# Kernel tuning notes

Measured on AMD Instinct MI355X. Metric: run time of the kernel, lower is better.

The kernel has to match this reference:

```python
import jax, jax.numpy as jnp
import numpy as np

B, T, C, H = 4, 4096, 1024, 64


def setup_inputs() -> dict:
    key = jax.random.key(0)
    k1, k2, k3, k4 = jax.random.split(key, 4)
    x = jax.random.normal(k1, (B, T, C), dtype=jnp.float32)
    # nn.Linear(C, H, bias=False) weights, stored as [C, H] so y = x @ W
    Wq = jax.random.normal(k2, (C, H), dtype=jnp.float32) * (C ** -0.5)
    Wk = jax.random.normal(k3, (C, H), dtype=jnp.float32) * (C ** -0.5)
    Wv = jax.random.normal(k4, (C, H), dtype=jnp.float32) * (C ** -0.5)
    return {"x": x, "Wq": Wq, "Wk": Wk, "Wv": Wv}


def reference(x, Wq, Wk, Wv):
    # x: (B,T,C) -> q,k,v: (B,T,H)
    q = jnp.einsum('btc,ch->bth', x, Wq)
    k = jnp.einsum('btc,ch->bth', x, Wk)
    v = jnp.einsum('btc,ch->bth', x, Wv)
    scale = q.shape[-1] ** -0.5
    # (B,T,T) attention scores with causal mask
    scores = jnp.einsum('bqh,bkh->bqk', q, k) * scale
    t = x.shape[1]
    causal = jnp.tril(jnp.ones((t, t), dtype=bool))
    scores = jnp.where(causal, scores, -jnp.inf)
    attn = jax.nn.softmax(scores, axis=-1)
    return jnp.einsum('bqk,bkh->bqh', attn, v)
```

## Files before the change

### kernel.cpp

```cpp
#include <hip/hip_runtime.h>

#define BATCH 4
#define SEQ   4096
#define CDIM  1024
#define HDIM  64

typedef __attribute__((ext_vector_type(8))) short bf16x8;
typedef __attribute__((ext_vector_type(4))) float f32x4;

#define WT_OFF 0
#define Q_OFF  (3 * HDIM * CDIM)
#define KF_OFF (Q_OFF + BATCH * SEQ * HDIM)
#define VF_OFF (KF_OFF + BATCH * SEQ * HDIM)

static __device__ __forceinline__ short f2bf(float f) {
  union { float f; unsigned u; } a; a.f = f;
  unsigned r = a.u + 0x7fffu + ((a.u >> 16) & 1u);
  return (short)(r >> 16);
}

static __device__ __forceinline__ bf16x8 ld8(const short* p) {
  return *(const bf16x8*)p;
}

__global__ void wcvt_kernel(const float* __restrict__ wq, const float* __restrict__ wk,
                            const float* __restrict__ wv, short* __restrict__ wt2) {
  int idx = blockIdx.x * 256 + threadIdx.x;
  int m = idx >> 16;
  int f = idx & 65535;
  int k0g = f >> 11, hc = (f >> 9) & 3, lr = (f >> 5) & 15, lg = (f >> 3) & 3, j = f & 7;
  int c = k0g * 32 + lg * 8 + j, h = hc * 16 + lr;
  const float* w = (m == 0) ? wq : (m == 1) ? wk : wv;
  wt2[((k0g * 12 + m * 4 + hc) * 64 + lr * 4 + lg) * 8 + j] = f2bf(w[c * 64 + h]);
}

__global__ __launch_bounds__(512) void proj_kernel(const float* __restrict__ x,
                                                   const short* __restrict__ wt2,
                                                   short* __restrict__ ws) {
  __shared__ short xs[2][1024];
  __shared__ short k_lds[8][16][24];
  __shared__ short v_lds[8][16][24];

  int tid = threadIdx.x;
  int widx = tid >> 6, lane = tid & 63;
  int lr = lane & 15, lg = lane >> 4;
  int row0 = blockIdx.x * 32;
  int rbh = widx >> 2;
  int hcw = widx & 3;

  int srow = tid >> 4, sc2 = tid & 15;
  const float* xsrc = x + (size_t)(row0 + srow) * CDIM + sc2 * 2;
  int sdst = (srow >> 4) * 512 + (srow & 15) * 32 + (sc2 >> 2) * 8 + (sc2 & 3) * 2;

  const short* xrd  = &xs[0][0] + rbh * 512 + (lr * 4 + lg) * 8;
  const short* bptr = wt2 + (hcw * 64 + lr * 4 + lg) * 8;

  f32x4 acc[3] = {};

#define LDX(K)  (*(const float2*)(xsrc + (K) * 32))
#define STAGE(A, BUF) do {                                                   \
    unsigned u_ = (unsigned)(unsigned short)f2bf((A).x) |                    \
                  ((unsigned)(unsigned short)f2bf((A).y) << 16);             \
    *(unsigned*)(&xs[(BUF)][sdst]) = u_;                                     \
  } while (0)
#define COMPUTE(BUF, K) do {                                                 \
    bf16x8 af_ = *(const bf16x8*)(xrd + (BUF) * 1024);                       \
    const short* bk_ = bptr + (K) * (12 * 512);                              \
    _Pragma("unroll")                                                        \
    for (int pp = 0; pp < 3; ++pp) {                                         \
      bf16x8 bf_ = ld8(bk_ + pp * 2048);                                     \
      acc[pp] = __builtin_amdgcn_mfma_f32_16x16x32_bf16(af_, bf_, acc[pp], 0, 0, 0); \
    }                                                                        \
  } while (0)

  float2 a1 = LDX(1);
  { float2 a0 = LDX(0); STAGE(a0, 0); }
  __syncthreads();

  for (int k = 0; k < 32; k += 2) {
    float2 an0 = {0.f, 0.f}, an1 = {0.f, 0.f};
    if (k + 2 < 32) an0 = LDX(k + 2);
    COMPUTE(0, k);
    STAGE(a1, 1);
    __syncthreads();
    if (k + 2 < 32) an1 = LDX(k + 3);
    COMPUTE(1, k + 1);
    if (k + 2 < 32) STAGE(an0, 0);
    __syncthreads();
    a1 = an1;
  }

  short* qs  = ws + Q_OFF;
  short* kfr = ws + KF_OFF;
  short* vfr = ws + VF_OFF;
  int rbase = row0 + rbh * 16;
#pragma unroll
  for (int reg = 0; reg < 4; ++reg) {
    int t = rbase + lg * 4 + reg;
    qs[t * 64 + hcw * 16 + lr] = f2bf(acc[0][reg]);
    k_lds[widx][lg * 4 + reg][lr] = f2bf(acc[1][reg]);
    v_lds[widx][lr][lg * 4 + reg] = f2bf(acc[2][reg]);
  }
  int b = rbase >> 12;
  int tb = rbase & (SEQ - 1);
  int kb64 = tb >> 6, st = (tb >> 4) & 3;
  if (lane < 32) {
    int i0 = lane >> 1, f8 = (lane & 1) * 8;
    size_t kblk = ((((size_t)b * 64 + kb64) * 4 + st) * 2 + (hcw >> 1)) * 512;
    bf16x8 kv8 = *(const bf16x8*)(&k_lds[widx][i0][f8]);
    *(bf16x8*)(kfr + kblk + ((hcw & 1) * 2 + (f8 >> 3)) * 128 + i0 * 8) = kv8;
    size_t vblk = ((((size_t)b * 64 + kb64) * 2 + ((tb >> 5) & 1)) * 4 + hcw) * 512;
    bf16x8 vv8 = *(const bf16x8*)(&v_lds[widx][i0][f8]);
    *(bf16x8*)(vfr + vblk + (((tb & 16) + f8) >> 3) * 128 + i0 * 8) = vv8;
  }
}

__global__ __launch_bounds__(512, 4) void attn_kernel(const short* __restrict__ ws,
                                                      float* __restrict__ out) {
  __shared__ float p_o[8][4][4][64];
  __shared__ float p_l[8][4][64];
  __shared__ short plds[8][16][72];

  int widx = threadIdx.x >> 6, lane = threadIdx.x & 63;
  int lr = lane & 15, lg = lane >> 4;
  int g = blockIdx.x;

  const short* qs  = ws + Q_OFF;
  const short* kfr = ws + KF_OFF;
  const short* vfr = ws + VF_OFF;
  short* myp = &plds[widx][0][0];

  for (int tt = 0; tt < 2; ++tt) {
    int j = tt == 0 ? g : 1023 - g;
    int t16 = 255 - (j >> 2), b = j & 3;
    int qrow0 = b * SEQ + t16 * 16;
    int nkv = (t16 >> 2) + 1;

    bf16x8 qf0 = ld8(qs + (qrow0 + lr) * 64 + lg * 8);
    bf16x8 qf1 = ld8(qs + (qrow0 + lr) * 64 + 32 + lg * 8);
    const short* kb_b = kfr + (size_t)b * 64 * 4096 + lane * 8;
    const short* vb_b = vfr + (size_t)b * 64 * 4096 + lane * 8;

    f32x4 o[4] = {};
    float l_run[4] = {};

    if (tt) __syncthreads();

    bf16x8 kf[8];
    int kvb = widx;
    if (kvb < nkv) {
      const short* kb = kb_b + (size_t)kvb * 4096;
#pragma unroll
      for (int q8 = 0; q8 < 8; ++q8) kf[q8] = ld8(kb + q8 * 512);
    }

    for (; kvb < nkv; kvb += 8) {
      int kv0 = kvb * 64;

      f32x4 s[4] = {};
#pragma unroll
      for (int st = 0; st < 4; ++st) {
        s[st] = __builtin_amdgcn_mfma_f32_16x16x32_bf16(qf0, kf[st * 2],     s[st], 0, 0, 0);
        s[st] = __builtin_amdgcn_mfma_f32_16x16x32_bf16(qf1, kf[st * 2 + 1], s[st], 0, 0, 0);
      }

      bf16x8 vv[8];
      {
        const short* vb = vb_b + (size_t)kvb * 4096;
#pragma unroll
        for (int q8 = 0; q8 < 8; ++q8) vv[q8] = ld8(vb + q8 * 512);
      }
      int kvn = kvb + 8;
      if (kvn < nkv) {
        const short* kb = kb_b + (size_t)kvn * 4096;
#pragma unroll
        for (int q8 = 0; q8 < 8; ++q8) kf[q8] = ld8(kb + q8 * 512);
      }

      bool last = (kvb == nkv - 1);
#pragma unroll
      for (int reg = 0; reg < 4; ++reg) {
        int ig = t16 * 16 + lg * 4 + reg;
#pragma unroll
        for (int st = 0; st < 4; ++st) {
          float v = s[st][reg] * 0.125f;
          if (last && (kv0 + st * 16 + lr > ig)) v = -1e30f;
          float p = __expf(v);
          l_run[reg] += p;
          myp[(lg * 4 + reg) * 72 + st * 16 + lr] = f2bf(p);
        }
      }
      asm volatile("s_waitcnt lgkmcnt(0)" ::: "memory");
      bf16x8 pf0 = ld8(myp + lr * 72 + lg * 8);
      bf16x8 pf1 = ld8(myp + lr * 72 + 32 + lg * 8);

#pragma unroll
      for (int hc = 0; hc < 4; ++hc) {
        o[hc] = __builtin_amdgcn_mfma_f32_16x16x32_bf16(pf0, vv[hc],     o[hc], 0, 0, 0);
        o[hc] = __builtin_amdgcn_mfma_f32_16x16x32_bf16(pf1, vv[4 + hc], o[hc], 0, 0, 0);
      }
    }

#pragma unroll
    for (int reg = 0; reg < 4; ++reg) {
      float l = l_run[reg];
      l += __shfl_xor(l, 1);
      l += __shfl_xor(l, 2);
      l += __shfl_xor(l, 4);
      l += __shfl_xor(l, 8);
      l_run[reg] = l;
    }

#pragma unroll
    for (int hc = 0; hc < 4; ++hc)
#pragma unroll
      for (int reg = 0; reg < 4; ++reg)
        p_o[widx][hc][reg][lane] = o[hc][reg];
#pragma unroll
    for (int reg = 0; reg < 4; ++reg)
      p_l[widx][reg][lane] = l_run[reg];
    __syncthreads();

    if (widx < 4) {
      int reg = widx;
      float lsum = 0.f;
#pragma unroll
      for (int w = 0; w < 8; ++w) lsum += p_l[w][reg][lane];
      float inv = 1.0f / lsum;
#pragma unroll
      for (int hc = 0; hc < 4; ++hc) {
        float sv = 0.f;
#pragma unroll
        for (int w = 0; w < 8; ++w) sv += p_o[w][hc][reg][lane];
        out[(qrow0 + lg * 4 + reg) * 64 + hc * 16 + lr] = sv * inv;
      }
    }
  }
}

extern "C" void kernel_launch(void* const* d_in, const int* in_sizes, int n_in,
                              void* d_out, int out_size, void* d_ws, size_t ws_size,
                              hipStream_t stream) {
  const float* x  = (const float*)d_in[0];
  const float* wq = (const float*)d_in[1];
  const float* wk = (const float*)d_in[2];
  const float* wv = (const float*)d_in[3];
  short* ws = (short*)d_ws;
  float* out = (float*)d_out;

  wcvt_kernel<<<dim3(768), dim3(256), 0, stream>>>(wq, wk, wv, ws + WT_OFF);
  proj_kernel<<<dim3(512), dim3(512), 0, stream>>>(x, ws + WT_OFF, ws);
  attn_kernel<<<dim3(512), dim3(512), 0, stream>>>(ws, out);
}
```

Before: 65.25 us.

## Stage x in 256-wide chunks with XOR-swizzled LDS and fewer barriers

```diff
diff --git a/kernel.cpp b/kernel.cpp
--- a/kernel.cpp
+++ b/kernel.cpp
@@ -34,10 +34,10 @@
   wt2[((k0g * 12 + m * 4 + hc) * 64 + lr * 4 + lg) * 8 + j] = f2bf(w[c * 64 + h]);
 }
 
-__global__ __launch_bounds__(512) void proj_kernel(const float* __restrict__ x,
-                                                   const short* __restrict__ wt2,
-                                                   short* __restrict__ ws) {
-  __shared__ short xs[2][1024];
+__global__ __launch_bounds__(512, 4) void proj_kernel(const float* __restrict__ x,
+                                                      const short* __restrict__ wt2,
+                                                      short* __restrict__ ws) {
+  __shared__ short xs2[2][32 * 256];
   __shared__ short k_lds[8][16][24];
   __shared__ short v_lds[8][16][24];
 
@@ -48,46 +48,67 @@
   int rbh = widx >> 2;
   int hcw = widx & 3;
 
-  int srow = tid >> 4, sc2 = tid & 15;
-  const float* xsrc = x + (size_t)(row0 + srow) * CDIM + sc2 * 2;
-  int sdst = (srow >> 4) * 512 + (srow & 15) * 32 + (sc2 >> 2) * 8 + (sc2 & 3) * 2;
-
-  const short* xrd  = &xs[0][0] + rbh * 512 + (lr * 4 + lg) * 8;
+  int sr = tid >> 4, sci = tid & 15;
+  const float* xsrc = x + (size_t)(row0 + sr) * CDIM + sci * 4;
+  int sxor = (sr & 7) << 4;
+  int sbase = sr * 512;
+
+  int rowa = rbh * 16 + lr;
+  int abase = rowa * 512;
+  int axor = (rowa & 7) << 4;
+
   const short* bptr = wt2 + (hcw * 64 + lr * 4 + lg) * 8;
 
   f32x4 acc[3] = {};
 
-#define LDX(K)  (*(const float2*)(xsrc + (K) * 32))
-#define STAGE(A, BUF) do {                                                   \
-    unsigned u_ = (unsigned)(unsigned short)f2bf((A).x) |                    \
-                  ((unsigned)(unsigned short)f2bf((A).y) << 16);             \
-    *(unsigned*)(&xs[(BUF)][sdst]) = u_;                                     \
+#define PLOAD(RG, P) do {                                                    \
+    _Pragma("unroll")                                                        \
+    for (int q = 0; q < 4; ++q)                                              \
+      RG[q] = *(const float4*)(xsrc + (P) * 256 + q * 64);                   \
   } while (0)
-#define COMPUTE(BUF, K) do {                                                 \
-    bf16x8 af_ = *(const bf16x8*)(xrd + (BUF) * 1024);                       \
-    const short* bk_ = bptr + (K) * (12 * 512);                              \
+
+#define PSTORE(RG, BUF) do {                                                 \
+    char* bc_ = (char*)&xs2[(BUF)][0];                                       \
     _Pragma("unroll")                                                        \
-    for (int pp = 0; pp < 3; ++pp) {                                         \
-      bf16x8 bf_ = ld8(bk_ + pp * 2048);                                     \
-      acc[pp] = __builtin_amdgcn_mfma_f32_16x16x32_bf16(af_, bf_, acc[pp], 0, 0, 0); \
+    for (int q = 0; q < 4; ++q) {                                            \
+      uint2 u_;                                                              \
+      u_.x = (unsigned)(unsigned short)f2bf(RG[q].x) |                       \
+             ((unsigned)(unsigned short)f2bf(RG[q].y) << 16);                \
+      u_.y = (unsigned)(unsigned short)f2bf(RG[q].z) |                       \
+             ((unsigned)(unsigned short)f2bf(RG[q].w) << 16);                \
+      *(uint2*)(bc_ + sbase + ((sci * 8 + q * 128) ^ sxor)) = u_;            \
     }                                                                        \
   } while (0)
 
-  float2 a1 = LDX(1);
-  { float2 a0 = LDX(0); STAGE(a0, 0); }
+#define PCOMPUTE(BUF, P) do {                                                \
+    const char* bufc_ = (const char*)&xs2[(BUF)][0];                         \
+    _Pragma("unroll")                                                        \
+    for (int kk = 0; kk < 8; ++kk) {                                         \
+      bf16x8 af_ = *(const bf16x8*)(bufc_ + abase + ((kk * 64 + lg * 16) ^ axor)); \
+      const short* bk_ = bptr + ((P) * 8 + kk) * 6144;                       \
+      _Pragma("unroll")                                                      \
+      for (int m = 0; m < 3; ++m) {                                          \
+        bf16x8 bf_ = ld8(bk_ + m * 2048);                                    \
+        acc[m] = __builtin_amdgcn_mfma_f32_16x16x32_bf16(af_, bf_, acc[m], 0, 0, 0); \
+      }                                                                      \
+    }                                                                        \
+  } while (0)
+
+  {
+    float4 rg[4];
+    PLOAD(rg, 0);
+    PSTORE(rg, 0);
+  }
   __syncthreads();
-
-  for (int k = 0; k < 32; k += 2) {
-    float2 an0 = {0.f, 0.f}, an1 = {0.f, 0.f};
-    if (k + 2 < 32) an0 = LDX(k + 2);
-    COMPUTE(0, k);
-    STAGE(a1, 1);
-    __syncthreads();
-    if (k + 2 < 32) an1 = LDX(k + 3);
-    COMPUTE(1, k + 1);
-    if (k + 2 < 32) STAGE(an0, 0);
-    __syncthreads();
-    a1 = an1;
+#pragma unroll
+  for (int p = 0; p < 4; ++p) {
+    float4 rg[4];
+    if (p < 3) PLOAD(rg, p + 1);
+    PCOMPUTE(p & 1, p);
+    if (p < 3) {
+      PSTORE(rg, (p + 1) & 1);
+      __syncthreads();
+    }
   }
 
   short* qs  = ws + Q_OFF;
```

Result: slower. 67.30 us (+3.1%).

## Stage full x row tile in LDS once and reuse weight fragments across rows

Applied to the files above, without the earlier changes.

```diff
diff --git a/kernel.cpp b/kernel.cpp
--- a/kernel.cpp
+++ b/kernel.cpp
@@ -8,15 +8,21 @@
 typedef __attribute__((ext_vector_type(8))) short bf16x8;
 typedef __attribute__((ext_vector_type(4))) float f32x4;
 
-#define WT_OFF 0
-#define Q_OFF  (3 * HDIM * CDIM)
-#define KF_OFF (Q_OFF + BATCH * SEQ * HDIM)
-#define VF_OFF (KF_OFF + BATCH * SEQ * HDIM)
+#define WT_OFF  0
+#define Q_OFF   (3 * HDIM * CDIM)
+#define KF_OFF  (Q_OFF + BATCH * SEQ * HDIM)
+#define VF_OFF  (KF_OFF + BATCH * SEQ * HDIM)
 
 static __device__ __forceinline__ short f2bf(float f) {
   union { float f; unsigned u; } a; a.f = f;
   unsigned r = a.u + 0x7fffu + ((a.u >> 16) & 1u);
   return (short)(r >> 16);
+}
+
+static __device__ __forceinline__ unsigned cvtpk(float lo, float hi) {
+  unsigned r;
+  asm("v_cvt_pk_bf16_f32 %0, %1, %2" : "=v"(r) : "v"(lo), "v"(hi));
+  return r;
 }
 
 static __device__ __forceinline__ bf16x8 ld8(const short* p) {
@@ -34,84 +40,85 @@
   wt2[((k0g * 12 + m * 4 + hc) * 64 + lr * 4 + lg) * 8 + j] = f2bf(w[c * 64 + h]);
 }
 
-__global__ __launch_bounds__(512) void proj_kernel(const float* __restrict__ x,
-                                                   const short* __restrict__ wt2,
-                                                   short* __restrict__ ws) {
-  __shared__ short xs[2][1024];
-  __shared__ short k_lds[8][16][24];
-  __shared__ short v_lds[8][16][24];
+__global__ __launch_bounds__(256, 2) void proj_kernel(const float* __restrict__ x,
+                                                      const short* __restrict__ wt2,
+                                                      short* __restrict__ ws) {
+  __shared__ short xc[32 * 1024];
+  __shared__ short k_lds[4][2][16][16];
+  __shared__ short v_lds[4][2][16][16];
 
   int tid = threadIdx.x;
-  int widx = tid >> 6, lane = tid & 63;
+  int w = tid >> 6, lane = tid & 63;
   int lr = lane & 15, lg = lane >> 4;
   int row0 = blockIdx.x * 32;
-  int rbh = widx >> 2;
-  int hcw = widx & 3;
-
-  int srow = tid >> 4, sc2 = tid & 15;
-  const float* xsrc = x + (size_t)(row0 + srow) * CDIM + sc2 * 2;
-  int sdst = (srow >> 4) * 512 + (srow & 15) * 32 + (sc2 >> 2) * 8 + (sc2 & 3) * 2;
-
-  const short* xrd  = &xs[0][0] + rbh * 512 + (lr * 4 + lg) * 8;
-  const short* bptr = wt2 + (hcw * 64 + lr * 4 + lg) * 8;
-
-  f32x4 acc[3] = {};
-
-#define LDX(K)  (*(const float2*)(xsrc + (K) * 32))
-#define STAGE(A, BUF) do {                                                   \
-    unsigned u_ = (unsigned)(unsigned short)f2bf((A).x) |                    \
-                  ((unsigned)(unsigned short)f2bf((A).y) << 16);             \
-    *(unsigned*)(&xs[(BUF)][sdst]) = u_;                                     \
-  } while (0)
-#define COMPUTE(BUF, K) do {                                                 \
-    bf16x8 af_ = *(const bf16x8*)(xrd + (BUF) * 1024);                       \
-    const short* bk_ = bptr + (K) * (12 * 512);                              \
-    _Pragma("unroll")                                                        \
-    for (int pp = 0; pp < 3; ++pp) {                                         \
-      bf16x8 bf_ = ld8(bk_ + pp * 2048);                                     \
-      acc[pp] = __builtin_amdgcn_mfma_f32_16x16x32_bf16(af_, bf_, acc[pp], 0, 0, 0); \
-    }                                                                        \
-  } while (0)
-
-  float2 a1 = LDX(1);
-  { float2 a0 = LDX(0); STAGE(a0, 0); }
+
+  {
+    int r = tid >> 3, t8 = tid & 7;
+    const float* xrow = x + (size_t)(row0 + r) * CDIM;
+    char* xcb = (char*)xc + r * 2048;
+    int rx = (r & 7) << 4;
+#pragma unroll
+    for (int j = 0; j < 16; ++j) {
+      int c0 = t8 * 8 + j * 64;
+      float4 f1 = *(const float4*)(xrow + c0);
+      float4 f2 = *(const float4*)(xrow + c0 + 4);
+      union { unsigned u[4]; bf16x8 v; } o;
+      o.u[0] = cvtpk(f1.x, f1.y); o.u[1] = cvtpk(f1.z, f1.w);
+      o.u[2] = cvtpk(f2.x, f2.y); o.u[3] = cvtpk(f2.z, f2.w);
+      int slot = t8 + j * 8;
+      *(bf16x8*)(xcb + ((slot * 16) ^ rx)) = o.v;
+    }
+  }
   __syncthreads();
 
-  for (int k = 0; k < 32; k += 2) {
-    float2 an0 = {0.f, 0.f}, an1 = {0.f, 0.f};
-    if (k + 2 < 32) an0 = LDX(k + 2);
-    COMPUTE(0, k);
-    STAGE(a1, 1);
-    __syncthreads();
-    if (k + 2 < 32) an1 = LDX(k + 3);
-    COMPUTE(1, k + 1);
-    if (k + 2 < 32) STAGE(an0, 0);
-    __syncthreads();
-    a1 = an1;
+  const char* xcb = (const char*)xc;
+  int axor = (lr & 7) << 4;
+  const short* bptr = wt2 + w * 512 + (lr * 4 + lg) * 8;
+
+  f32x4 acc[3][2] = {};
+#pragma unroll 8
+  for (int kk = 0; kk < 32; ++kk) {
+    int co = (kk * 64 + lg * 16) ^ axor;
+    bf16x8 a0 = *(const bf16x8*)(xcb + lr * 2048 + co);
+    bf16x8 a1 = *(const bf16x8*)(xcb + (16 + lr) * 2048 + co);
+    const short* bk = bptr + kk * 6144;
+#pragma unroll
+    for (int m = 0; m < 3; ++m) {
+      bf16x8 bf = ld8(bk + m * 2048);
+      acc[m][0] = __builtin_amdgcn_mfma_f32_16x16x32_bf16(a0, bf, acc[m][0], 0, 0, 0);
+      acc[m][1] = __builtin_amdgcn_mfma_f32_16x16x32_bf16(a1, bf, acc[m][1], 0, 0, 0);
+    }
   }
 
   short* qs  = ws + Q_OFF;
   short* kfr = ws + KF_OFF;
   short* vfr = ws + VF_OFF;
-  int rbase = row0 + rbh * 16;
-#pragma unroll
-  for (int reg = 0; reg < 4; ++reg) {
-    int t = rbase + lg * 4 + reg;
-    qs[t * 64 + hcw * 16 + lr] = f2bf(acc[0][reg]);
-    k_lds[widx][lg * 4 + reg][lr] = f2bf(acc[1][reg]);
-    v_lds[widx][lr][lg * 4 + reg] = f2bf(acc[2][reg]);
-  }
-  int b = rbase >> 12;
-  int tb = rbase & (SEQ - 1);
-  int kb64 = tb >> 6, st = (tb >> 4) & 3;
+  int hcw = w;
+
+#pragma unroll
+  for (int rt = 0; rt < 2; ++rt) {
+    int rbase = row0 + rt * 16;
+#pragma unroll
+    for (int reg = 0; reg < 4; ++reg) {
+      qs[(rbase + lg * 4 + reg) * 64 + hcw * 16 + lr] = f2bf(acc[0][rt][reg]);
+      k_lds[hcw][rt][lg * 4 + reg][lr] = f2bf(acc[1][rt][reg]);
+      v_lds[hcw][rt][lr][lg * 4 + reg] = f2bf(acc[2][rt][reg]);
+    }
+  }
   if (lane < 32) {
     int i0 = lane >> 1, f8 = (lane & 1) * 8;
-    size_t kblk = ((((size_t)b * 64 + kb64) * 4 + st) * 2 + (hcw >> 1)) * 512;
-    bf16x8 kv8 = *(const bf16x8*)(&k_lds[widx][i0][f8]);
-    *(bf16x8*)(kfr + kblk + ((hcw & 1) * 2 + (f8 >> 3)) * 128 + i0 * 8) = kv8;
-    size_t vblk = ((((size_t)b * 64 + kb64) * 2 + ((tb >> 5) & 1)) * 4 + hcw) * 512;
-    bf16x8 vv8 = *(const bf16x8*)(&v_lds[widx][i0][f8]);
-    *(bf16x8*)(vfr + vblk + (((tb & 16) + f8) >> 3) * 128 + i0 * 8) = vv8;
+#pragma unroll
+    for (int rt = 0; rt < 2; ++rt) {
+      int rbase = row0 + rt * 16;
+      int b = rbase >> 12, tb = rbase & (SEQ - 1);
+      int kb64 = tb >> 6, st = (tb >> 4) & 3;
+      size_t kblk = ((((size_t)b * 64 + kb64) * 4 + st) * 2 + (hcw >> 1)) * 512;
+      bf16x8 kv8 = *(const bf16x8*)(&k_lds[hcw][rt][i0][f8]);
+      *(bf16x8*)(kfr + kblk + ((hcw & 1) * 2 + (f8 >> 3)) * 128 + i0 * 8) = kv8;
+      size_t vblk = ((((size_t)b * 64 + kb64) * 2 + ((tb >> 5) & 1)) * 4 + hcw) * 512;
+      bf16x8 vv8 = *(const bf16x8*)(&v_lds[hcw][rt][i0][f8]);
+      *(bf16x8*)(vfr + vblk + (((tb & 16) + f8) >> 3) * 128 + i0 * 8) = vv8;
+    }
   }
 }
 
@@ -225,13 +232,13 @@
       int reg = widx;
       float lsum = 0.f;
 #pragma unroll
-      for (int w = 0; w < 8; ++w) lsum += p_l[w][reg][lane];
+      for (int w2 = 0; w2 < 8; ++w2) lsum += p_l[w2][reg][lane];
       float inv = 1.0f / lsum;
 #pragma unroll
       for (int hc = 0; hc < 4; ++hc) {
         float sv = 0.f;
 #pragma unroll
-        for (int w = 0; w < 8; ++w) sv += p_o[w][hc][reg][lane];
+        for (int w2 = 0; w2 < 8; ++w2) sv += p_o[w2][hc][reg][lane];
         out[(qrow0 + lg * 4 + reg) * 64 + hc * 16 + lr] = sv * inv;
       }
     }
@@ -249,6 +256,6 @@
   float* out = (float*)d_out;
 
   wcvt_kernel<<<dim3(768), dim3(256), 0, stream>>>(wq, wk, wv, ws + WT_OFF);
-  proj_kernel<<<dim3(512), dim3(512), 0, stream>>>(x, ws + WT_OFF, ws);
+  proj_kernel<<<dim3(512), dim3(256), 0, stream>>>(x, ws + WT_OFF, ws);
   attn_kernel<<<dim3(512), dim3(512), 0, stream>>>(ws, out);
 }
```

Result: faster. 62.91 us (-3.6%).
